# Kernel optimization log

Measured on AMD Instinct MI355X. Metric: run time of the kernel, lower is better.

Reference implementation:

```python
import jax, jax.numpy as jnp
import numpy as np

N_NODES = 100000
N_EDGES = 1600000
DIM_IN = 128
DIM_OUT = 128


def setup_inputs() -> dict:
    key = jax.random.key(0)
    k_x, k_w, k_r, k_c, k_v = jax.random.split(key, 5)
    x = jax.random.normal(k_x, (N_NODES, DIM_IN), dtype=jnp.float32)
    # Linear(dim_in, dim_out, bias=False): weight is [dim_out, dim_in]
    W = jax.random.normal(k_w, (DIM_OUT, DIM_IN), dtype=jnp.float32) * (1.0 / np.sqrt(DIM_IN))
    edge_row = jax.random.randint(k_r, (N_EDGES,), 0, N_NODES, dtype=jnp.int32)
    edge_col = jax.random.randint(k_c, (N_EDGES,), 0, N_NODES, dtype=jnp.int32)
    edge_val = jax.random.uniform(k_v, (N_EDGES,), dtype=jnp.float32)
    return {"x": x, "W": W, "edge_row": edge_row, "edge_col": edge_col, "edge_val": edge_val}


def reference(x, W, edge_row, edge_col, edge_val):
    # h = x @ W.T   (Linear, no bias)  -> [N, dim_out]
    h = jnp.einsum('nd,od->no', x, W)
    # SpMM: out[i] = sum_{e: row[e]==i} val[e] * h[col[e]]
    msgs = edge_val[:, None] * h[edge_col]          # [E, dim_out] irregular gather
    out = jax.ops.segment_sum(msgs, edge_row, num_segments=N_NODES)  # scatter-add
    return out
```

## Files before the change

kernel.cpp:

```cpp
#include <hip/hip_runtime.h>

#define DIM 128
#define CAP 48

typedef __bf16 bf16x8 __attribute__((ext_vector_type(8)));
typedef __bf16 bf16x2 __attribute__((ext_vector_type(2)));
typedef float  f32x4  __attribute__((ext_vector_type(4)));

__global__ __launch_bounds__(256) void prep(const float* __restrict__ W,
                                            __bf16* __restrict__ Wb,
                                            int* __restrict__ cursors,
                                            int n_nodes) {
    int i = blockIdx.x * 256 + threadIdx.x;
    if (i < DIM * DIM) Wb[i] = (__bf16)W[i];
    int j = i - DIM * DIM;
    if (j >= 0 && j < n_nodes) cursors[j] = 0;
}

__global__ __launch_bounds__(256) void gemm_and_bucket(
    const float* __restrict__ x, const __bf16* __restrict__ Wb,
    __bf16* __restrict__ hb, int n_nodes,
    const int* __restrict__ er, const int* __restrict__ ec,
    const float* __restrict__ ev, int* __restrict__ cursors,
    unsigned* __restrict__ buckets, int n_edges, int n_gemm_blocks) {

    if ((int)blockIdx.x < n_gemm_blocks) {
        const int wave = threadIdx.x >> 6;
        const int lane = threadIdx.x & 63;
        const int m = lane & 15, q = lane >> 4;
        const int nodebase = blockIdx.x * 64 + wave * 16;
        int rowA = nodebase + m;
        if (rowA >= n_nodes) rowA = n_nodes - 1;

        f32x4 acc[8];
#pragma unroll
        for (int t = 0; t < 8; ++t) acc[t] = (f32x4){0.f, 0.f, 0.f, 0.f};

#pragma unroll
        for (int s = 0; s < 4; ++s) {
            const float* xp = x + (size_t)rowA * DIM + s * 32 + q * 8;
            float4 xa = *(const float4*)xp;
            float4 xb = *(const float4*)(xp + 4);
            bf16x8 a;
            a[0] = (__bf16)xa.x; a[1] = (__bf16)xa.y;
            a[2] = (__bf16)xa.z; a[3] = (__bf16)xa.w;
            a[4] = (__bf16)xb.x; a[5] = (__bf16)xb.y;
            a[6] = (__bf16)xb.z; a[7] = (__bf16)xb.w;
#pragma unroll
            for (int t = 0; t < 8; ++t) {
                bf16x8 b = *(const bf16x8*)(Wb + (size_t)(t * 16 + m) * DIM + s * 32 + q * 8);
                acc[t] = __builtin_amdgcn_mfma_f32_16x16x32_bf16(a, b, acc[t], 0, 0, 0);
            }
        }
#pragma unroll
        for (int reg = 0; reg < 4; ++reg) {
            int r = nodebase + q * 4 + reg;
            if (r < n_nodes) {
                __bf16* hp = hb + (size_t)r * DIM + m;
#pragma unroll
                for (int t = 0; t < 8; ++t)
                    hp[t * 16] = (__bf16)acc[t][reg];
            }
        }
    } else {
        const int bb = blockIdx.x - n_gemm_blocks;
        const int chunk = bb >> 3;
        const int g = blockIdx.x & 7;
        const int lo = (int)(((long long)n_nodes * g) >> 3);
        const int hi = (int)(((long long)n_nodes * (g + 1)) >> 3);
        const int base = (chunk * 256 + (int)threadIdx.x) * 4;
        if (base >= n_edges) return;
        int4   r4 = *(const int4*)(er + base);
        int4   c4 = *(const int4*)(ec + base);
        float4 v4 = *(const float4*)(ev + base);
        const int   rr[4] = {r4.x, r4.y, r4.z, r4.w};
        const int   cc[4] = {c4.x, c4.y, c4.z, c4.w};
        const float vv[4] = {v4.x, v4.y, v4.z, v4.w};
#pragma unroll
        for (int j = 0; j < 4; ++j) {
            if (rr[j] >= lo && rr[j] < hi) {
                int slot = atomicAdd(&cursors[rr[j]], 1);
                if (slot < CAP) {
                    unsigned q = (unsigned)(vv[j] * 32768.f + 0.5f);
                    if (q > 32767u) q = 32767u;
                    buckets[(size_t)rr[j] * CAP + slot] = (q << 17) | (unsigned)cc[j];
                }
            }
        }
    }
}

__global__ __launch_bounds__(256) void segment_reduce(
    const unsigned* __restrict__ buckets, const int* __restrict__ cursors,
    const __bf16* __restrict__ hb, float* __restrict__ out,
    const int* __restrict__ er, const int* __restrict__ ec,
    const float* __restrict__ ev, int n_edges, int n_nodes) {

    const int rs = threadIdx.x >> 6;
    const int f  = threadIdx.x & 63;
    const int r  = blockIdx.x * 4 + rs;
    __shared__ int   sc[4][CAP];
    __shared__ float sv[4][CAP];

    const bool valid = r < n_nodes;
    const int ncur = valid ? cursors[r] : 0;
    const int n = (ncur > CAP) ? 0 : ncur;
    if (valid && f < n) {
        unsigned p = buckets[(size_t)r * CAP + f];
        sc[rs][f] = (int)(p & 0x1FFFFu);
        sv[rs][f] = (float)(p >> 17) * (1.f / 32768.f);
    }
    __syncthreads();
    if (!valid) return;

    float2 acc = make_float2(0.f, 0.f);
    if (ncur <= CAP) {
        int j = 0;
        for (; j + 8 <= n; j += 8) {
            bf16x2 hreg[8];
            float  vreg[8];
#pragma unroll
            for (int u = 0; u < 8; ++u) {
                vreg[u] = sv[rs][j + u];
                hreg[u] = *(const bf16x2*)(hb + (size_t)sc[rs][j + u] * DIM + 2 * f);
            }
#pragma unroll
            for (int u = 0; u < 8; ++u) {
                acc.x += vreg[u] * (float)hreg[u][0];
                acc.y += vreg[u] * (float)hreg[u][1];
            }
        }
        for (; j < n; ++j) {
            float v = sv[rs][j];
            bf16x2 h2 = *(const bf16x2*)(hb + (size_t)sc[rs][j] * DIM + 2 * f);
            acc.x += v * (float)h2[0];
            acc.y += v * (float)h2[1];
        }
    } else {
        for (int e = 0; e < n_edges; ++e) {
            if (er[e] == r) {
                float v = ev[e];
                bf16x2 h2 = *(const bf16x2*)(hb + (size_t)ec[e] * DIM + 2 * f);
                acc.x += v * (float)h2[0];
                acc.y += v * (float)h2[1];
            }
        }
    }
    *(float2*)(out + (size_t)r * DIM + 2 * f) = acc;
}

extern "C" void kernel_launch(void* const* d_in, const int* in_sizes, int n_in,
                              void* d_out, int out_size, void* d_ws, size_t ws_size,
                              hipStream_t stream) {
    const float* x  = (const float*)d_in[0];
    const float* W  = (const float*)d_in[1];
    const int*   er = (const int*)d_in[2];
    const int*   ec = (const int*)d_in[3];
    const float* ev = (const float*)d_in[4];
    float* out = (float*)d_out;

    const int n_nodes = in_sizes[0] / DIM;
    const int n_edges = in_sizes[2];

    char* wsb = (char*)d_ws;
    __bf16* Wb = (__bf16*)wsb;
    __bf16* hb = (__bf16*)(wsb + 32768);
    unsigned* buckets = (unsigned*)(wsb + 32768 + (size_t)n_nodes * DIM * 2);
    int* cursors = (int*)(wsb + 32768 + (size_t)n_nodes * DIM * 2 +
                          (size_t)n_nodes * CAP * 4);

    const int prep_items = DIM * DIM + n_nodes;
    prep<<<(prep_items + 255) / 256, 256, 0, stream>>>(W, Wb, cursors, n_nodes);

    const int n_gemm_blocks = (n_nodes + 63) / 64;
    const int n_chunks = (n_edges + 1023) / 1024;
    const int n_bucket_blocks = n_chunks * 8;
    gemm_and_bucket<<<n_gemm_blocks + n_bucket_blocks, 256, 0, stream>>>(
        x, Wb, hb, n_nodes, er, ec, ev, cursors, buckets, n_edges, n_gemm_blocks);

    segment_reduce<<<(n_nodes + 3) / 4, 256, 0, stream>>>(
        buckets, cursors, hb, out, er, ec, ev, n_edges, n_nodes);
}
```

Before: 268.4 us.

## Split segment-reduce wave into two edge halves with 8-byte gathers; nontemporal input loads

The segment-reduce kernel now has each wave split into two 32-lane halves. Each half processes alternate edges and loads 4 bf16 features (8 bytes) per lane instead of 2, and the halves are combined with a cross-half shuffle before the store. The edge lists are zero-padded to an even length, which makes the gathers wider and gives each wave two independent rows in flight. Separately, the x and edge-array streaming loads use nontemporal loads to avoid polluting cache that the gather relies on. The cost is a shuffle reduction, and idle half-waves on the rare overflow path.

```diff
diff --git a/kernel.cpp b/kernel.cpp
--- a/kernel.cpp
+++ b/kernel.cpp
@@ -4,8 +4,12 @@
 #define CAP 48
 
 typedef __bf16 bf16x8 __attribute__((ext_vector_type(8)));
-typedef __bf16 bf16x2 __attribute__((ext_vector_type(2)));
+typedef __bf16 bf16x4 __attribute__((ext_vector_type(4)));
 typedef float  f32x4  __attribute__((ext_vector_type(4)));
+typedef int    i32x4  __attribute__((ext_vector_type(4)));
+
+template <typename T>
+__device__ __forceinline__ T ntload(const T* p) { return __builtin_nontemporal_load(p); }
 
 __global__ __launch_bounds__(256) void prep(const float* __restrict__ W,
                                             __bf16* __restrict__ Wb,
@@ -39,13 +43,11 @@
 #pragma unroll
         for (int s = 0; s < 4; ++s) {
             const float* xp = x + (size_t)rowA * DIM + s * 32 + q * 8;
-            float4 xa = *(const float4*)xp;
-            float4 xb = *(const float4*)(xp + 4);
+            f32x4 xa = ntload((const f32x4*)xp);
+            f32x4 xb = ntload((const f32x4*)(xp + 4));
             bf16x8 a;
-            a[0] = (__bf16)xa.x; a[1] = (__bf16)xa.y;
-            a[2] = (__bf16)xa.z; a[3] = (__bf16)xa.w;
-            a[4] = (__bf16)xb.x; a[5] = (__bf16)xb.y;
-            a[6] = (__bf16)xb.z; a[7] = (__bf16)xb.w;
+#pragma unroll
+            for (int u = 0; u < 4; ++u) { a[u] = (__bf16)xa[u]; a[4 + u] = (__bf16)xb[u]; }
 #pragma unroll
             for (int t = 0; t < 8; ++t) {
                 bf16x8 b = *(const bf16x8*)(Wb + (size_t)(t * 16 + m) * DIM + s * 32 + q * 8);
@@ -70,20 +72,18 @@
         const int hi = (int)(((long long)n_nodes * (g + 1)) >> 3);
         const int base = (chunk * 256 + (int)threadIdx.x) * 4;
         if (base >= n_edges) return;
-        int4   r4 = *(const int4*)(er + base);
-        int4   c4 = *(const int4*)(ec + base);
-        float4 v4 = *(const float4*)(ev + base);
-        const int   rr[4] = {r4.x, r4.y, r4.z, r4.w};
-        const int   cc[4] = {c4.x, c4.y, c4.z, c4.w};
-        const float vv[4] = {v4.x, v4.y, v4.z, v4.w};
+        i32x4 r4 = ntload((const i32x4*)(er + base));
+        i32x4 c4 = ntload((const i32x4*)(ec + base));
+        f32x4 v4 = ntload((const f32x4*)(ev + base));
 #pragma unroll
         for (int j = 0; j < 4; ++j) {
-            if (rr[j] >= lo && rr[j] < hi) {
-                int slot = atomicAdd(&cursors[rr[j]], 1);
+            int rr = r4[j];
+            if (rr >= lo && rr < hi) {
+                int slot = atomicAdd(&cursors[rr], 1);
                 if (slot < CAP) {
-                    unsigned q = (unsigned)(vv[j] * 32768.f + 0.5f);
+                    unsigned q = (unsigned)(v4[j] * 32768.f + 0.5f);
                     if (q > 32767u) q = 32767u;
-                    buckets[(size_t)rr[j] * CAP + slot] = (q << 17) | (unsigned)cc[j];
+                    buckets[(size_t)rr * CAP + slot] = (q << 17) | (unsigned)c4[j];
                 }
             }
         }
@@ -96,57 +96,70 @@
     const int* __restrict__ er, const int* __restrict__ ec,
     const float* __restrict__ ev, int n_edges, int n_nodes) {
 
-    const int rs = threadIdx.x >> 6;
-    const int f  = threadIdx.x & 63;
-    const int r  = blockIdx.x * 4 + rs;
+    const int w    = threadIdx.x >> 6;
+    const int lane = threadIdx.x & 63;
+    const int sub  = lane & 31;
+    const int epair = lane >> 5;
+    const int r = blockIdx.x * 4 + w;
     __shared__ int   sc[4][CAP];
     __shared__ float sv[4][CAP];
 
     const bool valid = r < n_nodes;
     const int ncur = valid ? cursors[r] : 0;
     const int n = (ncur > CAP) ? 0 : ncur;
-    if (valid && f < n) {
-        unsigned p = buckets[(size_t)r * CAP + f];
-        sc[rs][f] = (int)(p & 0x1FFFFu);
-        sv[rs][f] = (float)(p >> 17) * (1.f / 32768.f);
+    if (valid && lane < CAP) {
+        if (lane < n) {
+            unsigned p = buckets[(size_t)r * CAP + lane];
+            sc[w][lane] = (int)(p & 0x1FFFFu);
+            sv[w][lane] = (float)(p >> 17) * (1.f / 32768.f);
+        } else {
+            sc[w][lane] = 0;
+            sv[w][lane] = 0.f;
+        }
     }
     __syncthreads();
     if (!valid) return;
 
-    float2 acc = make_float2(0.f, 0.f);
+    f32x4 acc = (f32x4){0.f, 0.f, 0.f, 0.f};
     if (ncur <= CAP) {
+        const int nn = (n + 1) & ~1;
         int j = 0;
-        for (; j + 8 <= n; j += 8) {
-            bf16x2 hreg[8];
-            float  vreg[8];
+        for (; j + 8 <= nn; j += 8) {
+            bf16x4 hreg[4];
+            float  vreg[4];
 #pragma unroll
-            for (int u = 0; u < 8; ++u) {
-                vreg[u] = sv[rs][j + u];
-                hreg[u] = *(const bf16x2*)(hb + (size_t)sc[rs][j + u] * DIM + 2 * f);
+            for (int u = 0; u < 4; ++u) {
+                const int idx = j + 2 * u + epair;
+                vreg[u] = sv[w][idx];
+                hreg[u] = *(const bf16x4*)(hb + (size_t)sc[w][idx] * DIM + sub * 4);
             }
 #pragma unroll
-            for (int u = 0; u < 8; ++u) {
-                acc.x += vreg[u] * (float)hreg[u][0];
-                acc.y += vreg[u] * (float)hreg[u][1];
-            }
+            for (int u = 0; u < 4; ++u)
+#pragma unroll
+                for (int k = 0; k < 4; ++k)
+                    acc[k] += vreg[u] * (float)hreg[u][k];
         }
-        for (; j < n; ++j) {
-            float v = sv[rs][j];
-            bf16x2 h2 = *(const bf16x2*)(hb + (size_t)sc[rs][j] * DIM + 2 * f);
-            acc.x += v * (float)h2[0];
-            acc.y += v * (float)h2[1];
+        for (; j < nn; j += 2) {
+            const int idx = j + epair;
+            const float v = sv[w][idx];
+            bf16x4 h4 = *(const bf16x4*)(hb + (size_t)sc[w][idx] * DIM + sub * 4);
+#pragma unroll
+            for (int k = 0; k < 4; ++k) acc[k] += v * (float)h4[k];
         }
-    } else {
+    } else if (epair == 0) {
         for (int e = 0; e < n_edges; ++e) {
             if (er[e] == r) {
-                float v = ev[e];
-                bf16x2 h2 = *(const bf16x2*)(hb + (size_t)ec[e] * DIM + 2 * f);
-                acc.x += v * (float)h2[0];
-                acc.y += v * (float)h2[1];
+                const float v = ev[e];
+                bf16x4 h4 = *(const bf16x4*)(hb + (size_t)ec[e] * DIM + sub * 4);
+#pragma unroll
+                for (int k = 0; k < 4; ++k) acc[k] += v * (float)h4[k];
             }
         }
     }
-    *(float2*)(out + (size_t)r * DIM + 2 * f) = acc;
+#pragma unroll
+    for (int k = 0; k < 4; ++k) acc[k] += __shfl_down(acc[k], 32);
+    if (epair == 0)
+        *(f32x4*)(out + (size_t)r * DIM + sub * 4) = acc;
 }
 
 extern "C" void kernel_launch(void* const* d_in, const int* in_sizes, int n_in,
```

After: 266.8 us. Within noise of the previous version (-0.6%).
